# Performance work log

Measured on AMD Instinct MI355X. Metric: run time of the kernel, lower is better.

Reference implementation:

```python
import jax, jax.numpy as jnp
import numpy as np

DIM = 1024
N_HEAD = 16
HEAD_DIM = DIM // N_HEAD
B, T = 2, 2048


def setup_inputs() -> dict:
    key = jax.random.key(0)
    ks = jax.random.split(key, 9)
    s = 1.0 / np.sqrt(DIM)
    return {
        "x": jax.random.normal(ks[0], (B, T, DIM), dtype=jnp.float32),
        "Wq": jax.random.normal(ks[1], (DIM, DIM), dtype=jnp.float32) * s,
        "bq": jax.random.normal(ks[2], (DIM,), dtype=jnp.float32) * s,
        "Wk": jax.random.normal(ks[3], (DIM, DIM), dtype=jnp.float32) * s,
        "bk": jax.random.normal(ks[4], (DIM,), dtype=jnp.float32) * s,
        "Wv": jax.random.normal(ks[5], (DIM, DIM), dtype=jnp.float32) * s,
        "bv": jax.random.normal(ks[6], (DIM,), dtype=jnp.float32) * s,
        "Wo": jax.random.normal(ks[7], (DIM, DIM), dtype=jnp.float32) * s,
        "bo": jax.random.normal(ks[8], (DIM,), dtype=jnp.float32) * s,
    }


def reference(x, Wq, bq, Wk, bk, Wv, bv, Wo, bo):
    b, t, d = x.shape
    # torch nn.Linear: y = x @ W.T + b
    Q = x @ Wq.T + bq  # [b, t, d]
    K = x @ Wk.T + bk
    V = x @ Wv.T + bv
    # split heads -> [b, h, t, hd]
    Q = Q.reshape(b, t, N_HEAD, HEAD_DIM).transpose(0, 2, 1, 3)
    K = K.reshape(b, t, N_HEAD, HEAD_DIM).transpose(0, 2, 1, 3)
    V = V.reshape(b, t, N_HEAD, HEAD_DIM).transpose(0, 2, 1, 3)
    scale = 1.0 / jnp.sqrt(jnp.float32(HEAD_DIM))
    score = jnp.einsum('bhqd,bhkd->bhqk', Q, K) * scale  # [b, h, t, t]
    attn = jax.nn.softmax(score, axis=-1)
    # dropout is identity in eval mode
    out = jnp.einsum('bhqk,bhkd->bhqd', attn, V)  # [b, h, t, hd]
    out = out.transpose(0, 2, 1, 3).reshape(b, t, d)
    return out @ Wo.T + bo
```

## Files before the change

kernel.cpp:

```cpp
#include <hip/hip_runtime.h>


#define DIM 1024
#define NH 16
#define HD 64
#define SEQ 2048
#define NROWS 4096

typedef unsigned short u16;
typedef unsigned int u32;
typedef __bf16 bf16_t;
typedef bf16_t bf16x8 __attribute__((ext_vector_type(8)));
typedef float f32x4 __attribute__((ext_vector_type(4)));
typedef u16 u16x4 __attribute__((ext_vector_type(4)));
typedef u32 u32x2 __attribute__((ext_vector_type(2)));

typedef const __attribute__((address_space(1))) void* gas_ptr;
typedef __attribute__((address_space(3))) void* las_ptr;

#define S_BARRIER() asm volatile("s_barrier" ::: "memory")
#define S_WAITCNT_VM(N) asm volatile("s_waitcnt vmcnt(" #N ")" ::: "memory")

__device__ __forceinline__ void gl_lds16(const void* g, void* lds_wave_base) {
  __builtin_amdgcn_global_load_lds((gas_ptr)g, (las_ptr)lds_wave_base, 16, 0, 0);
}

__device__ __forceinline__ f32x4 mfma_bf16(bf16x8 a, bf16x8 b, f32x4 c) {
  return __builtin_amdgcn_mfma_f32_16x16x32_bf16(a, b, c, 0, 0, 0);
}

__device__ __forceinline__ u32 cvtpk(float lo, float hi) {
  u32 r;
  asm("v_cvt_pk_bf16_f32 %0, %1, %2" : "=v"(r) : "v"(lo), "v"(hi));
  return r;
}

__device__ __forceinline__ u16 bfu(float f) {
  bf16_t b = (bf16_t)f;
  union { bf16_t b; u16 u; } cv; cv.b = b; return cv.u;
}

__device__ __forceinline__ float fexp2(float x) {
#if __has_builtin(__builtin_amdgcn_exp2f)
  return __builtin_amdgcn_exp2f(x);
#else
  return exp2f(x);
#endif
}

#define QSCALE 0.18033688f

__global__ void cvt_all(const float* __restrict__ x,
                        const float* __restrict__ wq, const float* __restrict__ wk,
                        const float* __restrict__ wv, const float* __restrict__ wo,
                        u16* __restrict__ xb,
                        u16* __restrict__ oq, u16* __restrict__ ok,
                        u16* __restrict__ ov, u16* __restrict__ oo) {
  const int bid = blockIdx.x;
  const float* in;
  u16* out;
  float s = 1.0f;
  int off;
  if (bid < 4096) {
    in = x; out = xb; off = bid;
  } else {
    const int wi = (bid - 4096) >> 10;
    off = (bid - 4096) & 1023;
    in = wi == 0 ? wq : wi == 1 ? wk : wi == 2 ? wv : wo;
    out = wi == 0 ? oq : wi == 1 ? ok : wi == 2 ? ov : oo;
    if (wi == 0) s = QSCALE;
  }
  const int i = off * 256 + threadIdx.x;
  float4 v = ((const float4*)in)[i];
  u16x4 o;
  o.x = bfu(v.x * s); o.y = bfu(v.y * s); o.z = bfu(v.z * s); o.w = bfu(v.w * s);
  ((u16x4*)out)[i] = o;
}

__device__ __forceinline__ int xcd_swz(int L, int nwg) {
  return (L & 7) * (nwg >> 3) + (L >> 3);
}

__global__ __launch_bounds__(256, 3) void gemm_qkv(const u16* __restrict__ A,
                                                   const u16* __restrict__ wq,
                                                   const u16* __restrict__ wk,
                                                   const u16* __restrict__ wv,
                                                   const float* __restrict__ bq,
                                                   const float* __restrict__ bk,
                                                   const float* __restrict__ bv,
                                                   u16* __restrict__ Qb,
                                                   u16* __restrict__ Kb,
                                                   u16* __restrict__ Vtb) {
  __shared__ u16 As[2][128 * 32];
  __shared__ u16 Bs[2][128 * 32];
  const int L = blockIdx.y * gridDim.x + blockIdx.x;
  const int swz = xcd_swz(L, gridDim.x * gridDim.y);
  const int bx = swz % gridDim.x, by = swz / gridDim.x;
  const int which = bx >> 3;
  const int col0 = (bx & 7) * 128;
  const u16* W = which == 0 ? wq : which == 1 ? wk : wv;
  const float* bias = which == 0 ? bq : which == 1 ? bk : bv;
  const float bscale = which == 0 ? QSCALE : 1.0f;

  const int t = threadIdx.x, lane = t & 63, w = t >> 6;
  const int row0 = by * 128;
  const int wr = w >> 1, wc = w & 1;
  const int lr = lane & 15, lk = lane >> 4;

  f32x4 acc[4][4] = {};

  auto stage = [&](int k0, int bu) {
#pragma unroll
    for (int i = 0; i < 2; ++i) {
      const int bc = i * 256 + w * 64;
      const int f = bc + lane;
      gl_lds16(A + (size_t)(row0 + (f >> 2)) * DIM + k0 + (f & 3) * 8, &As[bu][bc * 8]);
      gl_lds16(W + (size_t)(col0 + (f >> 2)) * DIM + k0 + (f & 3) * 8, &Bs[bu][bc * 8]);
    }
  };

  stage(0, 0);
  int buf = 0;
  for (int k0 = 0; k0 < DIM; k0 += 32) {
    if (k0 + 32 < DIM) { stage(k0 + 32, buf ^ 1); S_WAITCNT_VM(4); }
    else               { S_WAITCNT_VM(0); }
    S_BARRIER();

    bf16x8 a[4], b[4];
#pragma unroll
    for (int m = 0; m < 4; ++m)
      a[m] = *(const bf16x8*)&As[buf][(wr * 64 + m * 16 + lr) * 32 + lk * 8];
#pragma unroll
    for (int n = 0; n < 4; ++n)
      b[n] = *(const bf16x8*)&Bs[buf][(wc * 64 + n * 16 + lr) * 32 + lk * 8];
    __builtin_amdgcn_s_setprio(1);
#pragma unroll
    for (int m = 0; m < 4; ++m)
#pragma unroll
      for (int n = 0; n < 4; ++n)
        acc[m][n] = mfma_bf16(a[m], b[n], acc[m][n]);
    __builtin_amdgcn_s_setprio(0);

    S_BARRIER();
    buf ^= 1;
  }

#pragma unroll
  for (int m = 0; m < 4; ++m) {
    const int rowb = row0 + wr * 64 + m * 16 + lk * 4;
#pragma unroll
    for (int n = 0; n < 4; ++n) {
      const int ocol = col0 + wc * 64 + n * 16 + lr;
      const float bc = bias[ocol] * bscale;
      if (which != 2) {
        u16* dst = which == 0 ? Qb : Kb;
#pragma unroll
        for (int r = 0; r < 4; ++r)
          dst[(size_t)(rowb + r) * DIM + ocol] = bfu(acc[m][n][r] + bc);
      } else {
        u16x4 pk;
#pragma unroll
        for (int r = 0; r < 4; ++r) pk[r] = bfu(acc[m][n][r] + bc);
        const size_t idx = ((((size_t)(rowb >> 11) * NH + (ocol >> 6)) * HD + (ocol & 63)) << 11) + (rowb & 2047);
        *(u16x4*)&Vtb[idx] = pk;
      }
    }
  }
}

__global__ __launch_bounds__(256, 2) void gemm_out(const u16* __restrict__ A,
                                                   const u16* __restrict__ W,
                                                   const float* __restrict__ bias,
                                                   float* __restrict__ C) {
  __shared__ u16 As[2][64 * 32];
  __shared__ u16 Bs[2][128 * 32];
  const int L = blockIdx.x;
  const int swz = xcd_swz(L, 512);
  const int row0 = (swz >> 3) * 64, col0 = (swz & 7) * 128;
  const int t = threadIdx.x, lane = t & 63, w = t >> 6;
  const int wr = w >> 1, wc = w & 1;
  const int lr = lane & 15, lk = lane >> 4;

  f32x4 acc[2][4] = {};

  auto stage = [&](int k0, int bu) {
    const int fa = w * 64 + lane;
    gl_lds16(A + (size_t)(row0 + (fa >> 2)) * DIM + k0 + (fa & 3) * 8, &As[bu][w * 512]);
#pragma unroll
    for (int i = 0; i < 2; ++i) {
      const int bc = i * 256 + w * 64;
      const int fb = bc + lane;
      gl_lds16(W + (size_t)(col0 + (fb >> 2)) * DIM + k0 + (fb & 3) * 8, &Bs[bu][bc * 8]);
    }
  };

  stage(0, 0);
  int buf = 0;
  for (int k0 = 0; k0 < DIM; k0 += 32) {
    if (k0 + 32 < DIM) { stage(k0 + 32, buf ^ 1); S_WAITCNT_VM(3); }
    else               { S_WAITCNT_VM(0); }
    S_BARRIER();

    bf16x8 a[2], b[4];
#pragma unroll
    for (int m = 0; m < 2; ++m)
      a[m] = *(const bf16x8*)&As[buf][(wr * 32 + m * 16 + lr) * 32 + lk * 8];
#pragma unroll
    for (int n = 0; n < 4; ++n)
      b[n] = *(const bf16x8*)&Bs[buf][(wc * 64 + n * 16 + lr) * 32 + lk * 8];
    __builtin_amdgcn_s_setprio(1);
#pragma unroll
    for (int m = 0; m < 2; ++m)
#pragma unroll
      for (int n = 0; n < 4; ++n)
        acc[m][n] = mfma_bf16(a[m], b[n], acc[m][n]);
    __builtin_amdgcn_s_setprio(0);

    S_BARRIER();
    buf ^= 1;
  }

#pragma unroll
  for (int m = 0; m < 2; ++m) {
    const int rowb = row0 + wr * 32 + m * 16 + lk * 4;
#pragma unroll
    for (int n = 0; n < 4; ++n) {
      const int col = col0 + wc * 64 + n * 16 + lr;
      const float bc = bias[col];
#pragma unroll
      for (int r = 0; r < 4; ++r)
        C[(size_t)(rowb + r) * DIM + col] = acc[m][n][r] + bc;
    }
  }
}

__global__ __launch_bounds__(256, 4) void flash_attn(const u16* __restrict__ Q,
                                                     const u16* __restrict__ K,
                                                     const u16* __restrict__ Vt,
                                                     u16* __restrict__ O) {
  __shared__ u16 Ks[2][64 * 64];
  __shared__ u16 Vs[2][64 * 64];
  __shared__ u16 Ps[4][16][64];

  const int t = threadIdx.x, lane = t & 63, w = t >> 6;
  const int L = blockIdx.x;
  const int bh = ((L >> 8) << 3) | (L & 7);
  const int qt = (L >> 3) & 31;
  const int b = bh >> 4, h = bh & 15;
  const int q0 = qt * 64;
  const int lr = lane & 15, lk = lane >> 4;

  const size_t qrow = (size_t)(b * SEQ + q0 + w * 16 + lr);
  bf16x8 qf[2];
  qf[0] = *(const bf16x8*)&Q[qrow * DIM + h * HD + lk * 8];
  qf[1] = *(const bf16x8*)&Q[qrow * DIM + h * HD + lk * 8 + 32];

  f32x4 o[4] = {};
  float l0 = 0.f;

  auto stage = [&](int kt, int bu) {
#pragma unroll
    for (int i = 0; i < 2; ++i) {
      const int bc = i * 256 + w * 64;
      const int f = bc + lane;
      const int row = f >> 3, c = f & 7;
      const int cs = c ^ (row & 7);
      gl_lds16(K + (size_t)(b * SEQ + kt + row) * DIM + h * HD + cs * 8, &Ks[bu][bc * 8]);
      gl_lds16(Vt + (((size_t)bh * HD + row) << 11) + kt + cs * 8, &Vs[bu][bc * 8]);
    }
  };

  stage(0, 0);
  int buf = 0;
  for (int kt = 0; kt < SEQ; kt += 64) {
    if (kt + 64 < SEQ) { stage(kt + 64, buf ^ 1); S_WAITCNT_VM(4); }
    else               { S_WAITCNT_VM(0); }
    S_BARRIER();

    const u16* ks = Ks[buf];
    const u16* vs = Vs[buf];

    f32x4 s[4] = {};
    __builtin_amdgcn_s_setprio(1);
#pragma unroll
    for (int n = 0; n < 4; ++n) {
      const int row = n * 16 + lr;
#pragma unroll
      for (int kk = 0; kk < 2; ++kk) {
        bf16x8 kf = *(const bf16x8*)&ks[row * 64 + (((lk + kk * 4) ^ (row & 7)) * 8)];
        s[n] = mfma_bf16(kf, qf[kk], s[n]);
      }
    }
    __builtin_amdgcn_s_setprio(0);

    float p[4][4];
#pragma unroll
    for (int n = 0; n < 4; ++n)
#pragma unroll
      for (int r = 0; r < 4; ++r) { p[n][r] = fexp2(s[n][r]); l0 += p[n][r]; }

    const int rx = (lr & 7) << 3;
#pragma unroll
    for (int n = 0; n < 4; ++n) {
      u32x2 d2;
      d2[0] = cvtpk(p[n][0], p[n][1]);
      d2[1] = cvtpk(p[n][2], p[n][3]);
      *(u32x2*)&Ps[w][lr][(n * 16 + lk * 4) ^ rx] = d2;
    }

    __builtin_amdgcn_s_setprio(1);
#pragma unroll
    for (int kk = 0; kk < 2; ++kk) {
      bf16x8 pa = *(const bf16x8*)&Ps[w][lr][(kk * 32 + lk * 8) ^ rx];
#pragma unroll
      for (int nd = 0; nd < 4; ++nd) {
        const int vrow = nd * 16 + lr;
        bf16x8 vf = *(const bf16x8*)&vs[vrow * 64 + (((lk + kk * 4) ^ (vrow & 7)) * 8)];
        o[nd] = mfma_bf16(pa, vf, o[nd]);
      }
    }
    __builtin_amdgcn_s_setprio(0);

    S_BARRIER();
    buf ^= 1;
  }

  l0 += __shfl_xor(l0, 16);
  l0 += __shfl_xor(l0, 32);
#pragma unroll
  for (int r = 0; r < 4; ++r) {
    const float inv = 1.f / __shfl(l0, lk * 4 + r);
    const size_t grow = (size_t)(b * SEQ + q0 + w * 16 + lk * 4 + r);
#pragma unroll
    for (int nd = 0; nd < 4; ++nd)
      O[grow * DIM + h * HD + nd * 16 + lr] = bfu(o[nd][r] * inv);
  }
}

extern "C" void kernel_launch(void* const* d_in, const int* in_sizes, int n_in,
                              void* d_out, int out_size, void* d_ws, size_t ws_size,
                              hipStream_t stream) {
  (void)in_sizes; (void)n_in; (void)out_size; (void)ws_size;
  const float* x  = (const float*)d_in[0];
  const float* Wq = (const float*)d_in[1];
  const float* bq = (const float*)d_in[2];
  const float* Wk = (const float*)d_in[3];
  const float* bk = (const float*)d_in[4];
  const float* Wv = (const float*)d_in[5];
  const float* bv = (const float*)d_in[6];
  const float* Wo = (const float*)d_in[7];
  const float* bo = (const float*)d_in[8];

  char* ws = (char*)d_ws;
  u16* xb  = (u16*)(ws + 0);
  u16* wqb = (u16*)(ws + 8388608);
  u16* wkb = (u16*)(ws + 10485760);
  u16* wvb = (u16*)(ws + 12582912);
  u16* wob = (u16*)(ws + 14680064);
  u16* Qb  = (u16*)(ws + 16777216);
  u16* Kb  = (u16*)(ws + 25165824);
  u16* Vtb = (u16*)(ws + 33554432);
  u16* Ob  = (u16*)(ws + 41943040);

  cvt_all<<<8192, 256, 0, stream>>>(x, Wq, Wk, Wv, Wo, xb, wqb, wkb, wvb, wob);

  gemm_qkv<<<dim3(24, NROWS / 128), 256, 0, stream>>>(xb, wqb, wkb, wvb, bq, bk, bv, Qb, Kb, Vtb);

  flash_attn<<<1024, 256, 0, stream>>>(Qb, Kb, Vtb, Ob);

  gemm_out<<<512, 256, 0, stream>>>(Ob, wob, bo, (float*)d_out);
}
```

Before: 118.6 us.

## Triple-buffer GEMM loads and software-pipeline QK with PV in flash attention

Both projection GEMMs move from double to triple buffering in LDS with a prefetch distance of two tiles, and the trailing barrier is replaced by a leading one. The attention kernel is software-pipelined: the next tile's QK^T MFMAs are issued before the current tile's exp and PV, using a three-slot V buffer. The softmax row sum is now computed with an MFMA against a ones vector instead of scalar adds plus shuffles. The aim is to hide global-load latency and keep MFMA units busy. In exchange it uses more LDS and registers, and attention occupancy is lowered from 4 to 3 blocks per CU.

Measured after the change: 128.4 us. 1.08x slower.

```diff
diff --git a/kernel.cpp b/kernel.cpp
--- a/kernel.cpp
+++ b/kernel.cpp
@@ -6,6 +6,7 @@
 #define HD 64
 #define SEQ 2048
 #define NROWS 4096
+#define NT 32
 
 typedef unsigned short u16;
 typedef unsigned int u32;
@@ -91,8 +92,8 @@
                                                    u16* __restrict__ Qb,
                                                    u16* __restrict__ Kb,
                                                    u16* __restrict__ Vtb) {
-  __shared__ u16 As[2][128 * 32];
-  __shared__ u16 Bs[2][128 * 32];
+  __shared__ u16 As[3][128 * 32];
+  __shared__ u16 Bs[3][128 * 32];
   const int L = blockIdx.y * gridDim.x + blockIdx.x;
   const int swz = xcd_swz(L, gridDim.x * gridDim.y);
   const int bx = swz % gridDim.x, by = swz / gridDim.x;
@@ -120,19 +121,22 @@
   };
 
   stage(0, 0);
-  int buf = 0;
-  for (int k0 = 0; k0 < DIM; k0 += 32) {
-    if (k0 + 32 < DIM) { stage(k0 + 32, buf ^ 1); S_WAITCNT_VM(4); }
-    else               { S_WAITCNT_VM(0); }
+  stage(32, 1);
+  int bcur = 0, bst = 2;
+  for (int k = 0; k < 32; ++k) {
+    S_BARRIER();
+    if (k + 2 < 32) { stage((k + 2) * 32, bst); S_WAITCNT_VM(8); }
+    else if (k + 1 < 32) { S_WAITCNT_VM(4); }
+    else { S_WAITCNT_VM(0); }
     S_BARRIER();
 
     bf16x8 a[4], b[4];
 #pragma unroll
     for (int m = 0; m < 4; ++m)
-      a[m] = *(const bf16x8*)&As[buf][(wr * 64 + m * 16 + lr) * 32 + lk * 8];
+      a[m] = *(const bf16x8*)&As[bcur][(wr * 64 + m * 16 + lr) * 32 + lk * 8];
 #pragma unroll
     for (int n = 0; n < 4; ++n)
-      b[n] = *(const bf16x8*)&Bs[buf][(wc * 64 + n * 16 + lr) * 32 + lk * 8];
+      b[n] = *(const bf16x8*)&Bs[bcur][(wc * 64 + n * 16 + lr) * 32 + lk * 8];
     __builtin_amdgcn_s_setprio(1);
 #pragma unroll
     for (int m = 0; m < 4; ++m)
@@ -141,8 +145,8 @@
         acc[m][n] = mfma_bf16(a[m], b[n], acc[m][n]);
     __builtin_amdgcn_s_setprio(0);
 
-    S_BARRIER();
-    buf ^= 1;
+    bcur = bcur == 2 ? 0 : bcur + 1;
+    bst = bst == 2 ? 0 : bst + 1;
   }
 
 #pragma unroll
@@ -172,8 +176,8 @@
                                                    const u16* __restrict__ W,
                                                    const float* __restrict__ bias,
                                                    float* __restrict__ C) {
-  __shared__ u16 As[2][64 * 32];
-  __shared__ u16 Bs[2][128 * 32];
+  __shared__ u16 As[3][64 * 32];
+  __shared__ u16 Bs[3][128 * 32];
   const int L = blockIdx.x;
   const int swz = xcd_swz(L, 512);
   const int row0 = (swz >> 3) * 64, col0 = (swz & 7) * 128;
@@ -195,19 +199,22 @@
   };
 
   stage(0, 0);
-  int buf = 0;
-  for (int k0 = 0; k0 < DIM; k0 += 32) {
-    if (k0 + 32 < DIM) { stage(k0 + 32, buf ^ 1); S_WAITCNT_VM(3); }
-    else               { S_WAITCNT_VM(0); }
+  stage(32, 1);
+  int bcur = 0, bst = 2;
+  for (int k = 0; k < 32; ++k) {
+    S_BARRIER();
+    if (k + 2 < 32) { stage((k + 2) * 32, bst); S_WAITCNT_VM(6); }
+    else if (k + 1 < 32) { S_WAITCNT_VM(3); }
+    else { S_WAITCNT_VM(0); }
     S_BARRIER();
 
     bf16x8 a[2], b[4];
 #pragma unroll
     for (int m = 0; m < 2; ++m)
-      a[m] = *(const bf16x8*)&As[buf][(wr * 32 + m * 16 + lr) * 32 + lk * 8];
+      a[m] = *(const bf16x8*)&As[bcur][(wr * 32 + m * 16 + lr) * 32 + lk * 8];
 #pragma unroll
     for (int n = 0; n < 4; ++n)
-      b[n] = *(const bf16x8*)&Bs[buf][(wc * 64 + n * 16 + lr) * 32 + lk * 8];
+      b[n] = *(const bf16x8*)&Bs[bcur][(wc * 64 + n * 16 + lr) * 32 + lk * 8];
     __builtin_amdgcn_s_setprio(1);
 #pragma unroll
     for (int m = 0; m < 2; ++m)
@@ -216,8 +223,8 @@
         acc[m][n] = mfma_bf16(a[m], b[n], acc[m][n]);
     __builtin_amdgcn_s_setprio(0);
 
-    S_BARRIER();
-    buf ^= 1;
+    bcur = bcur == 2 ? 0 : bcur + 1;
+    bst = bst == 2 ? 0 : bst + 1;
   }
 
 #pragma unroll
@@ -234,12 +241,12 @@
   }
 }
 
-__global__ __launch_bounds__(256, 4) void flash_attn(const u16* __restrict__ Q,
+__global__ __launch_bounds__(256, 3) void flash_attn(const u16* __restrict__ Q,
                                                      const u16* __restrict__ K,
                                                      const u16* __restrict__ Vt,
                                                      u16* __restrict__ O) {
   __shared__ u16 Ks[2][64 * 64];
-  __shared__ u16 Vs[2][64 * 64];
+  __shared__ u16 Vs[3][64 * 64];
   __shared__ u16 Ps[4][16][64];
 
   const int t = threadIdx.x, lane = t & 63, w = t >> 6;
@@ -255,32 +262,26 @@
   qf[0] = *(const bf16x8*)&Q[qrow * DIM + h * HD + lk * 8];
   qf[1] = *(const bf16x8*)&Q[qrow * DIM + h * HD + lk * 8 + 32];
 
+  bf16x8 ones;
+#pragma unroll
+  for (int j = 0; j < 8; ++j) ones[j] = (bf16_t)1.0f;
+
   f32x4 o[4] = {};
-  float l0 = 0.f;
-
-  auto stage = [&](int kt, int bu) {
-#pragma unroll
-    for (int i = 0; i < 2; ++i) {
-      const int bc = i * 256 + w * 64;
+  f32x4 lacc = {};
+
+  auto stage = [&](int kt, int kb, int vb) {
+#pragma unroll
+    for (int i2 = 0; i2 < 2; ++i2) {
+      const int bc = i2 * 256 + w * 64;
       const int f = bc + lane;
       const int row = f >> 3, c = f & 7;
       const int cs = c ^ (row & 7);
-      gl_lds16(K + (size_t)(b * SEQ + kt + row) * DIM + h * HD + cs * 8, &Ks[bu][bc * 8]);
-      gl_lds16(Vt + (((size_t)bh * HD + row) << 11) + kt + cs * 8, &Vs[bu][bc * 8]);
+      gl_lds16(K + (size_t)(b * SEQ + kt + row) * DIM + h * HD + cs * 8, &Ks[kb][bc * 8]);
+      gl_lds16(Vt + (((size_t)bh * HD + row) << 11) + kt + cs * 8, &Vs[vb][bc * 8]);
     }
   };
 
-  stage(0, 0);
-  int buf = 0;
-  for (int kt = 0; kt < SEQ; kt += 64) {
-    if (kt + 64 < SEQ) { stage(kt + 64, buf ^ 1); S_WAITCNT_VM(4); }
-    else               { S_WAITCNT_VM(0); }
-    S_BARRIER();
-
-    const u16* ks = Ks[buf];
-    const u16* vs = Vs[buf];
-
-    f32x4 s[4] = {};
+  auto qk = [&](const u16* ks, f32x4 (&s)[4]) {
     __builtin_amdgcn_s_setprio(1);
 #pragma unroll
     for (int n = 0; n < 4; ++n) {
@@ -292,14 +293,34 @@
       }
     }
     __builtin_amdgcn_s_setprio(0);
+  };
+
+  stage(0, 0, 0);
+  stage(64, 1, 1);
+  S_WAITCNT_VM(4);
+  S_BARRIER();
+  f32x4 scur[4] = {};
+  qk(Ks[0], scur);
+
+  int vb_pv = 0, vb_st = 2;
+  const int rx = (lr & 7) << 3;
+#pragma unroll 2
+  for (int i = 0; i < NT; ++i) {
+    S_BARRIER();
+    if (i + 2 < NT) { stage((i + 2) * 64, i & 1, vb_st); }
+    f32x4 snext[4] = {};
+    if (i + 1 < NT) {
+      if (i + 2 < NT) { S_WAITCNT_VM(4); } else { S_WAITCNT_VM(0); }
+      S_BARRIER();
+      qk(Ks[(i + 1) & 1], snext);
+    }
 
     float p[4][4];
 #pragma unroll
     for (int n = 0; n < 4; ++n)
 #pragma unroll
-      for (int r = 0; r < 4; ++r) { p[n][r] = fexp2(s[n][r]); l0 += p[n][r]; }
-
-    const int rx = (lr & 7) << 3;
+      for (int r = 0; r < 4; ++r) p[n][r] = fexp2(scur[n][r]);
+
 #pragma unroll
     for (int n = 0; n < 4; ++n) {
       u32x2 d2;
@@ -308,10 +329,12 @@
       *(u32x2*)&Ps[w][lr][(n * 16 + lk * 4) ^ rx] = d2;
     }
 
+    const u16* vs = Vs[vb_pv];
     __builtin_amdgcn_s_setprio(1);
 #pragma unroll
     for (int kk = 0; kk < 2; ++kk) {
       bf16x8 pa = *(const bf16x8*)&Ps[w][lr][(kk * 32 + lk * 8) ^ rx];
+      lacc = mfma_bf16(pa, ones, lacc);
 #pragma unroll
       for (int nd = 0; nd < 4; ++nd) {
         const int vrow = nd * 16 + lr;
@@ -321,15 +344,15 @@
     }
     __builtin_amdgcn_s_setprio(0);
 
-    S_BARRIER();
-    buf ^= 1;
-  }
-
-  l0 += __shfl_xor(l0, 16);
-  l0 += __shfl_xor(l0, 32);
+#pragma unroll
+    for (int n = 0; n < 4; ++n) scur[n] = snext[n];
+    vb_pv = vb_pv == 2 ? 0 : vb_pv + 1;
+    vb_st = vb_st == 2 ? 0 : vb_st + 1;
+  }
+
 #pragma unroll
   for (int r = 0; r < 4; ++r) {
-    const float inv = 1.f / __shfl(l0, lk * 4 + r);
+    const float inv = 1.f / lacc[r];
     const size_t grow = (size_t)(b * SEQ + q0 + w * 16 + lk * 4 + r);
 #pragma unroll
     for (int nd = 0; nd < 4; ++nd)
```
